# Performance work log

Hardware: AMD Instinct MI355X
Metric: run time of the kernel (lower is better)

Reference implementation:

```python
import jax, jax.numpy as jnp
import numpy as np


def _pairwise_sq_dists(p, t):
    # p: [N,3], t: [M,3] -> [N,M] squared euclidean distances
    # |p|^2 + |t|^2 - 2 p.t^T (avoids materializing [N,M,3])
    p2 = jnp.sum(p * p, axis=-1)  # [N]
    t2 = jnp.sum(t * t, axis=-1)  # [M]
    cross = jnp.einsum('nd,md->nm', p, t)  # [N,M]
    d = p2[:, None] + t2[None, :] - 2.0 * cross
    return jnp.maximum(d, 0.0)  # clamp tiny negatives from cancellation


def setup_inputs() -> dict:
    key = jax.random.key(0)
    k1, k2 = jax.random.split(key)
    N = 16384
    predict = jax.random.normal(k1, (1, N, 3), dtype=jnp.float32)
    target = jax.random.normal(k2, (1, N, 3), dtype=jnp.float32)
    return {"predict": predict, "target": target}


def reference(predict, target):
    # Faithful to forward: only the first batch element is used.
    p = predict[0]  # [N,3]
    t = target[0]   # [M,3]
    d = _pairwise_sq_dists(p, t)          # [N,M] squared distances
    dist1 = jnp.min(d, axis=1)            # nearest target for each predict pt
    dist2 = jnp.min(d, axis=0)            # nearest predict for each target pt
    loss = jnp.mean(dist1) + jnp.mean(dist2)
    return loss
```

## Files before the change

kernel.cpp:

```cpp
#include <hip/hip_runtime.h>


typedef short s16x8 __attribute__((ext_vector_type(8)));
typedef float f32x16 __attribute__((ext_vector_type(16)));

static __device__ __forceinline__ unsigned short f2bf(float f) {
    unsigned u = __float_as_uint(f);
    unsigned r = (u + 0x7FFFu + ((u >> 16) & 1u)) >> 16;
    return (unsigned short)r;
}
static __device__ __forceinline__ float bf2f(unsigned short h) {
    return __uint_as_float(((unsigned)h) << 16);
}
static __device__ __forceinline__ void split2(float v, unsigned short& h, unsigned short& l) {
    h = f2bf(v);
    l = f2bf(v - bf2f(h));
}

union Pack16 { unsigned short u[16]; uint4 v[2]; };

__global__ void prep_pack(const float* __restrict__ predict, const float* __restrict__ target,
                          unsigned short* __restrict__ ApP, unsigned short* __restrict__ BpP,
                          unsigned short* __restrict__ ApT, unsigned short* __restrict__ BpT,
                          int N)
{
    int i = blockIdx.x * blockDim.x + threadIdx.x;
    if (i >= 2 * N) return;
    const float* src = (i < N) ? predict : target;
    unsigned short* Ap = (i < N) ? ApP : ApT;
    unsigned short* Bp = (i < N) ? BpP : BpT;
    int j = (i < N) ? i : i - N;

    float x = src[3*j], y = src[3*j+1], z = src[3*j+2];
    float n2 = __builtin_fmaf(x, x, __builtin_fmaf(y, y, z*z));

    unsigned short xh,xl,yh,yl,zh,zl,nh,nl,qxh,qxl,qyh,qyl,qzh,qzl;
    split2(x, xh, xl); split2(y, yh, yl); split2(z, zh, zl); split2(n2, nh, nl);
    split2(-2.0f*x, qxh, qxl); split2(-2.0f*y, qyh, qyl); split2(-2.0f*z, qzh, qzl);
    const unsigned short one = f2bf(1.0f);

    Pack16 a, b;
    a.u[0]=xh; a.u[1]=xh; a.u[2]=xl; a.u[3]=xl;
    a.u[4]=yh; a.u[5]=yh; a.u[6]=yl; a.u[7]=yl;
    a.u[8]=zh; a.u[9]=zh; a.u[10]=zl; a.u[11]=zl;
    a.u[12]=nh; a.u[13]=nl; a.u[14]=one; a.u[15]=one;

    b.u[0]=qxh; b.u[1]=qxl; b.u[2]=qxh; b.u[3]=qxl;
    b.u[4]=qyh; b.u[5]=qyl; b.u[6]=qyh; b.u[7]=qyl;
    b.u[8]=qzh; b.u[9]=qzl; b.u[10]=qzh; b.u[11]=qzl;
    b.u[12]=one; b.u[13]=one; b.u[14]=nh; b.u[15]=nl;

    uint4* ad = (uint4*)(Ap + (size_t)j * 16);
    uint4* bd = (uint4*)(Bp + (size_t)j * 16);
    ad[0] = a.v[0]; ad[1] = a.v[1];
    bd[0] = b.v[0]; bd[1] = b.v[1];
}

#define CG 8

__global__ __launch_bounds__(256, 2) void chamfer_main(
    const unsigned short* __restrict__ ApP, const unsigned short* __restrict__ BpP,
    const unsigned short* __restrict__ ApT, const unsigned short* __restrict__ BpT,
    float* __restrict__ partials, int N)
{
    const int dir = blockIdx.z;
    const unsigned short* __restrict__ Ap = dir ? ApT : ApP;
    const unsigned short* __restrict__ Bp = dir ? BpP : BpT;
    float* __restrict__ pout = partials + (size_t)(dir * CG + blockIdx.y) * N;

    const int tid  = threadIdx.x;
    const int w    = tid >> 6;
    const int lane = tid & 63;
    const int lm   = lane & 31;
    const int lg   = lane >> 5;

    const int row0 = blockIdx.x * 256 + w * 64;

    const uint4* A4 = (const uint4*)Ap;
    s16x8 a0 = __builtin_bit_cast(s16x8, A4[(size_t)(row0      + lm) * 2 + lg]);
    s16x8 a1 = __builtin_bit_cast(s16x8, A4[(size_t)(row0 + 32 + lm) * 2 + lg]);

    float rm0[16], rm1[16];
    #pragma unroll
    for (int r = 0; r < 16; ++r) { rm0[r] = 3.0e38f; rm1[r] = 3.0e38f; }

    const f32x16 zc = {0.f,0.f,0.f,0.f,0.f,0.f,0.f,0.f,0.f,0.f,0.f,0.f,0.f,0.f,0.f,0.f};

    const int npt = N / CG;
    const int NT  = npt / 32;
    const uint4* bp = (const uint4*)Bp + (size_t)blockIdx.y * npt * 2 + lm * 2 + lg;

    uint4 c0 = bp[0];
    uint4 c1 = bp[64];
    const uint4* bnext = bp + 128;

    for (int t = 0; t < NT - 2; t += 2) {
        uint4 n0 = bnext[0];
        uint4 n1 = bnext[64];
        bnext += 128;
        s16x8 bA = __builtin_bit_cast(s16x8, c0);
        s16x8 bB = __builtin_bit_cast(s16x8, c1);
        f32x16 p0 = __builtin_amdgcn_mfma_f32_32x32x16_bf16(a0, bA, zc, 0, 0, 0);
        f32x16 q0 = __builtin_amdgcn_mfma_f32_32x32x16_bf16(a0, bB, zc, 0, 0, 0);
        f32x16 p1 = __builtin_amdgcn_mfma_f32_32x32x16_bf16(a1, bA, zc, 0, 0, 0);
        f32x16 q1 = __builtin_amdgcn_mfma_f32_32x32x16_bf16(a1, bB, zc, 0, 0, 0);
        #pragma unroll
        for (int r = 0; r < 16; ++r) {
            rm0[r] = fminf(fminf(rm0[r], p0[r]), q0[r]);
            rm1[r] = fminf(fminf(rm1[r], p1[r]), q1[r]);
        }
        c0 = n0; c1 = n1;
    }
    {
        s16x8 bA = __builtin_bit_cast(s16x8, c0);
        s16x8 bB = __builtin_bit_cast(s16x8, c1);
        f32x16 p0 = __builtin_amdgcn_mfma_f32_32x32x16_bf16(a0, bA, zc, 0, 0, 0);
        f32x16 q0 = __builtin_amdgcn_mfma_f32_32x32x16_bf16(a0, bB, zc, 0, 0, 0);
        f32x16 p1 = __builtin_amdgcn_mfma_f32_32x32x16_bf16(a1, bA, zc, 0, 0, 0);
        f32x16 q1 = __builtin_amdgcn_mfma_f32_32x32x16_bf16(a1, bB, zc, 0, 0, 0);
        #pragma unroll
        for (int r = 0; r < 16; ++r) {
            rm0[r] = fminf(fminf(rm0[r], p0[r]), q0[r]);
            rm1[r] = fminf(fminf(rm1[r], p1[r]), q1[r]);
        }
    }

    #pragma unroll
    for (int m = 1; m <= 16; m <<= 1) {
        #pragma unroll
        for (int r = 0; r < 16; ++r) {
            rm0[r] = fminf(rm0[r], __shfl_xor(rm0[r], m, 64));
            rm1[r] = fminf(rm1[r], __shfl_xor(rm1[r], m, 64));
        }
    }
    #pragma unroll
    for (int r = 0; r < 16; ++r) {
        int rl = (r & 3) + 8 * (r >> 2) + 4 * lg;
        if (lm == r) {
            pout[row0 +      rl] = rm0[r];
            pout[row0 + 32 + rl] = rm1[r];
        }
    }
}

__global__ void chamfer_reduce1(const float* __restrict__ partials,
                                double* __restrict__ bsum, int N)
{
    const int n4 = N >> 2;
    const float4* p4 = (const float4*)partials;
    double acc = 0.0;
    for (int i = blockIdx.x * blockDim.x + threadIdx.x; i < n4;
         i += gridDim.x * blockDim.x) {
        float4 m0 = p4[i];
        #pragma unroll
        for (int g = 1; g < CG; ++g) {
            float4 v = p4[(size_t)g * n4 + i];
            m0.x = fminf(m0.x, v.x); m0.y = fminf(m0.y, v.y);
            m0.z = fminf(m0.z, v.z); m0.w = fminf(m0.w, v.w);
        }
        float4 m1 = p4[(size_t)CG * n4 + i];
        #pragma unroll
        for (int g = CG + 1; g < 2 * CG; ++g) {
            float4 v = p4[(size_t)g * n4 + i];
            m1.x = fminf(m1.x, v.x); m1.y = fminf(m1.y, v.y);
            m1.z = fminf(m1.z, v.z); m1.w = fminf(m1.w, v.w);
        }
        acc += (double)fmaxf(m0.x, 0.0f) + (double)fmaxf(m0.y, 0.0f)
             + (double)fmaxf(m0.z, 0.0f) + (double)fmaxf(m0.w, 0.0f)
             + (double)fmaxf(m1.x, 0.0f) + (double)fmaxf(m1.y, 0.0f)
             + (double)fmaxf(m1.z, 0.0f) + (double)fmaxf(m1.w, 0.0f);
    }
    for (int off = 32; off; off >>= 1)
        acc += __shfl_down(acc, off, 64);
    __shared__ double sacc[4];
    const int wave = threadIdx.x >> 6, lane = threadIdx.x & 63;
    if (lane == 0) sacc[wave] = acc;
    __syncthreads();
    if (threadIdx.x == 0)
        bsum[blockIdx.x] = sacc[0] + sacc[1] + sacc[2] + sacc[3];
}

__global__ void chamfer_reduce2(const double* __restrict__ bsum,
                                float* __restrict__ out, int N, int nb)
{
    if (threadIdx.x == 0) {
        double t = 0.0;
        for (int i = 0; i < nb; ++i) t += bsum[i];
        out[0] = (float)(t / (double)N);
    }
}

extern "C" void kernel_launch(void* const* d_in, const int* in_sizes, int n_in,
                              void* d_out, int out_size, void* d_ws, size_t ws_size,
                              hipStream_t stream) {
    const float* predict = (const float*)d_in[0];
    const float* target  = (const float*)d_in[1];
    const int N = in_sizes[0] / 3;

    unsigned short* ws16 = (unsigned short*)d_ws;
    unsigned short* ApP = ws16;
    unsigned short* BpP = ws16 + (size_t)1 * N * 16;
    unsigned short* ApT = ws16 + (size_t)2 * N * 16;
    unsigned short* BpT = ws16 + (size_t)3 * N * 16;
    float* partials = (float*)(ws16 + (size_t)4 * N * 16);
    double* bsum = (double*)(partials + (size_t)2 * CG * N);

    prep_pack<<<dim3((2 * N + 255) / 256), dim3(256), 0, stream>>>(
        predict, target, ApP, BpP, ApT, BpT, N);

    dim3 grid(N / 256, CG, 2);
    chamfer_main<<<grid, dim3(256), 0, stream>>>(ApP, BpP, ApT, BpT, partials, N);

    chamfer_reduce1<<<dim3(16), dim3(256), 0, stream>>>(partials, bsum, N);
    chamfer_reduce2<<<dim3(1), dim3(64), 0, stream>>>(bsum, (float*)d_out, N, 16);
}
```

Before: 83.60 us.

## Fuse reductions into main kernel via atomicMin and last-block ticket

Drops the partials buffer and the two reduce kernels. Each block now atomicMins its clamped per-row minima, stored as uint bits, into a 2N array that prep_pack initialises, and the last block to finish (found with an atomic ticket) sums the array and writes the loss. The main loop is also unrolled to four B tiles per iteration with deeper prefetch. This cuts two kernel launches and the extra global traffic, at the cost of atomic contention, a serial final sum in one block, and higher register pressure.

New measurement: 146.6 us. 1.75x slower.

```diff
diff --git a/kernel.cpp b/kernel.cpp
--- a/kernel.cpp
+++ b/kernel.cpp
@@ -22,10 +22,14 @@
 __global__ void prep_pack(const float* __restrict__ predict, const float* __restrict__ target,
                           unsigned short* __restrict__ ApP, unsigned short* __restrict__ BpP,
                           unsigned short* __restrict__ ApT, unsigned short* __restrict__ BpT,
+                          unsigned* __restrict__ minbits, unsigned* __restrict__ ticket,
                           int N)
 {
     int i = blockIdx.x * blockDim.x + threadIdx.x;
+    if (i == 0) *ticket = 0u;
     if (i >= 2 * N) return;
+    minbits[i] = 0x7F7FFFFFu;
+
     const float* src = (i < N) ? predict : target;
     unsigned short* Ap = (i < N) ? ApP : ApT;
     unsigned short* Bp = (i < N) ? BpP : BpT;
@@ -61,12 +65,13 @@
 __global__ __launch_bounds__(256, 2) void chamfer_main(
     const unsigned short* __restrict__ ApP, const unsigned short* __restrict__ BpP,
     const unsigned short* __restrict__ ApT, const unsigned short* __restrict__ BpT,
-    float* __restrict__ partials, int N)
+    unsigned* __restrict__ minbits, unsigned* __restrict__ ticket,
+    float* __restrict__ out, int N)
 {
     const int dir = blockIdx.z;
     const unsigned short* __restrict__ Ap = dir ? ApT : ApP;
     const unsigned short* __restrict__ Bp = dir ? BpP : BpT;
-    float* __restrict__ pout = partials + (size_t)(dir * CG + blockIdx.y) * N;
+    unsigned* __restrict__ mout = minbits + (size_t)dir * N;
 
     const int tid  = threadIdx.x;
     const int w    = tid >> 6;
@@ -88,40 +93,69 @@
 
     const int npt = N / CG;
     const int NT  = npt / 32;
+    const int NQ  = NT / 4;
     const uint4* bp = (const uint4*)Bp + (size_t)blockIdx.y * npt * 2 + lm * 2 + lg;
 
-    uint4 c0 = bp[0];
-    uint4 c1 = bp[64];
-    const uint4* bnext = bp + 128;
-
-    for (int t = 0; t < NT - 2; t += 2) {
-        uint4 n0 = bnext[0];
-        uint4 n1 = bnext[64];
-        bnext += 128;
-        s16x8 bA = __builtin_bit_cast(s16x8, c0);
-        s16x8 bB = __builtin_bit_cast(s16x8, c1);
-        f32x16 p0 = __builtin_amdgcn_mfma_f32_32x32x16_bf16(a0, bA, zc, 0, 0, 0);
-        f32x16 q0 = __builtin_amdgcn_mfma_f32_32x32x16_bf16(a0, bB, zc, 0, 0, 0);
-        f32x16 p1 = __builtin_amdgcn_mfma_f32_32x32x16_bf16(a1, bA, zc, 0, 0, 0);
-        f32x16 q1 = __builtin_amdgcn_mfma_f32_32x32x16_bf16(a1, bB, zc, 0, 0, 0);
-        #pragma unroll
-        for (int r = 0; r < 16; ++r) {
-            rm0[r] = fminf(fminf(rm0[r], p0[r]), q0[r]);
-            rm1[r] = fminf(fminf(rm1[r], p1[r]), q1[r]);
-        }
-        c0 = n0; c1 = n1;
+    uint4 c0 = bp[0], c1 = bp[64], c2 = bp[128], c3 = bp[192];
+    const uint4* bn = bp + 256;
+
+    for (int t = 0; t < NQ - 1; ++t) {
+        uint4 n0 = bn[0], n1 = bn[64], n2 = bn[128], n3 = bn[192];
+        bn += 256;
+        {
+            s16x8 bA = __builtin_bit_cast(s16x8, c0);
+            s16x8 bB = __builtin_bit_cast(s16x8, c1);
+            f32x16 p0 = __builtin_amdgcn_mfma_f32_32x32x16_bf16(a0, bA, zc, 0, 0, 0);
+            f32x16 q0 = __builtin_amdgcn_mfma_f32_32x32x16_bf16(a0, bB, zc, 0, 0, 0);
+            f32x16 p1 = __builtin_amdgcn_mfma_f32_32x32x16_bf16(a1, bA, zc, 0, 0, 0);
+            f32x16 q1 = __builtin_amdgcn_mfma_f32_32x32x16_bf16(a1, bB, zc, 0, 0, 0);
+            #pragma unroll
+            for (int r = 0; r < 16; ++r) {
+                rm0[r] = fminf(fminf(rm0[r], p0[r]), q0[r]);
+                rm1[r] = fminf(fminf(rm1[r], p1[r]), q1[r]);
+            }
+        }
+        {
+            s16x8 bA = __builtin_bit_cast(s16x8, c2);
+            s16x8 bB = __builtin_bit_cast(s16x8, c3);
+            f32x16 p0 = __builtin_amdgcn_mfma_f32_32x32x16_bf16(a0, bA, zc, 0, 0, 0);
+            f32x16 q0 = __builtin_amdgcn_mfma_f32_32x32x16_bf16(a0, bB, zc, 0, 0, 0);
+            f32x16 p1 = __builtin_amdgcn_mfma_f32_32x32x16_bf16(a1, bA, zc, 0, 0, 0);
+            f32x16 q1 = __builtin_amdgcn_mfma_f32_32x32x16_bf16(a1, bB, zc, 0, 0, 0);
+            #pragma unroll
+            for (int r = 0; r < 16; ++r) {
+                rm0[r] = fminf(fminf(rm0[r], p0[r]), q0[r]);
+                rm1[r] = fminf(fminf(rm1[r], p1[r]), q1[r]);
+            }
+        }
+        c0 = n0; c1 = n1; c2 = n2; c3 = n3;
     }
     {
-        s16x8 bA = __builtin_bit_cast(s16x8, c0);
-        s16x8 bB = __builtin_bit_cast(s16x8, c1);
-        f32x16 p0 = __builtin_amdgcn_mfma_f32_32x32x16_bf16(a0, bA, zc, 0, 0, 0);
-        f32x16 q0 = __builtin_amdgcn_mfma_f32_32x32x16_bf16(a0, bB, zc, 0, 0, 0);
-        f32x16 p1 = __builtin_amdgcn_mfma_f32_32x32x16_bf16(a1, bA, zc, 0, 0, 0);
-        f32x16 q1 = __builtin_amdgcn_mfma_f32_32x32x16_bf16(a1, bB, zc, 0, 0, 0);
-        #pragma unroll
-        for (int r = 0; r < 16; ++r) {
-            rm0[r] = fminf(fminf(rm0[r], p0[r]), q0[r]);
-            rm1[r] = fminf(fminf(rm1[r], p1[r]), q1[r]);
+        {
+            s16x8 bA = __builtin_bit_cast(s16x8, c0);
+            s16x8 bB = __builtin_bit_cast(s16x8, c1);
+            f32x16 p0 = __builtin_amdgcn_mfma_f32_32x32x16_bf16(a0, bA, zc, 0, 0, 0);
+            f32x16 q0 = __builtin_amdgcn_mfma_f32_32x32x16_bf16(a0, bB, zc, 0, 0, 0);
+            f32x16 p1 = __builtin_amdgcn_mfma_f32_32x32x16_bf16(a1, bA, zc, 0, 0, 0);
+            f32x16 q1 = __builtin_amdgcn_mfma_f32_32x32x16_bf16(a1, bB, zc, 0, 0, 0);
+            #pragma unroll
+            for (int r = 0; r < 16; ++r) {
+                rm0[r] = fminf(fminf(rm0[r], p0[r]), q0[r]);
+                rm1[r] = fminf(fminf(rm1[r], p1[r]), q1[r]);
+            }
+        }
+        {
+            s16x8 bA = __builtin_bit_cast(s16x8, c2);
+            s16x8 bB = __builtin_bit_cast(s16x8, c3);
+            f32x16 p0 = __builtin_amdgcn_mfma_f32_32x32x16_bf16(a0, bA, zc, 0, 0, 0);
+            f32x16 q0 = __builtin_amdgcn_mfma_f32_32x32x16_bf16(a0, bB, zc, 0, 0, 0);
+            f32x16 p1 = __builtin_amdgcn_mfma_f32_32x32x16_bf16(a1, bA, zc, 0, 0, 0);
+            f32x16 q1 = __builtin_amdgcn_mfma_f32_32x32x16_bf16(a1, bB, zc, 0, 0, 0);
+            #pragma unroll
+            for (int r = 0; r < 16; ++r) {
+                rm0[r] = fminf(fminf(rm0[r], p0[r]), q0[r]);
+                rm1[r] = fminf(fminf(rm1[r], p1[r]), q1[r]);
+            }
         }
     }
 
@@ -137,57 +171,37 @@
     for (int r = 0; r < 16; ++r) {
         int rl = (r & 3) + 8 * (r >> 2) + 4 * lg;
         if (lm == r) {
-            pout[row0 +      rl] = rm0[r];
-            pout[row0 + 32 + rl] = rm1[r];
-        }
-    }
-}
-
-__global__ void chamfer_reduce1(const float* __restrict__ partials,
-                                double* __restrict__ bsum, int N)
-{
-    const int n4 = N >> 2;
-    const float4* p4 = (const float4*)partials;
+            atomicMin(&mout[row0 +      rl], __float_as_uint(fmaxf(rm0[r], 0.0f)));
+            atomicMin(&mout[row0 + 32 + rl], __float_as_uint(fmaxf(rm1[r], 0.0f)));
+        }
+    }
+
+    __threadfence();
+    __shared__ unsigned is_last;
+    if (tid == 0) {
+        unsigned total = gridDim.x * gridDim.y * gridDim.z;
+        unsigned old = atomicAdd(ticket, 1u);
+        is_last = (old == total - 1u) ? 1u : 0u;
+    }
+    __syncthreads();
+    if (!is_last) return;
+    __threadfence();
+
+    const uint4* mb4 = (const uint4*)minbits;
+    const int n4 = (2 * N) >> 2;
     double acc = 0.0;
-    for (int i = blockIdx.x * blockDim.x + threadIdx.x; i < n4;
-         i += gridDim.x * blockDim.x) {
-        float4 m0 = p4[i];
-        #pragma unroll
-        for (int g = 1; g < CG; ++g) {
-            float4 v = p4[(size_t)g * n4 + i];
-            m0.x = fminf(m0.x, v.x); m0.y = fminf(m0.y, v.y);
-            m0.z = fminf(m0.z, v.z); m0.w = fminf(m0.w, v.w);
-        }
-        float4 m1 = p4[(size_t)CG * n4 + i];
-        #pragma unroll
-        for (int g = CG + 1; g < 2 * CG; ++g) {
-            float4 v = p4[(size_t)g * n4 + i];
-            m1.x = fminf(m1.x, v.x); m1.y = fminf(m1.y, v.y);
-            m1.z = fminf(m1.z, v.z); m1.w = fminf(m1.w, v.w);
-        }
-        acc += (double)fmaxf(m0.x, 0.0f) + (double)fmaxf(m0.y, 0.0f)
-             + (double)fmaxf(m0.z, 0.0f) + (double)fmaxf(m0.w, 0.0f)
-             + (double)fmaxf(m1.x, 0.0f) + (double)fmaxf(m1.y, 0.0f)
-             + (double)fmaxf(m1.z, 0.0f) + (double)fmaxf(m1.w, 0.0f);
+    for (int i = tid; i < n4; i += 256) {
+        uint4 v = mb4[i];
+        acc += (double)__uint_as_float(v.x) + (double)__uint_as_float(v.y)
+             + (double)__uint_as_float(v.z) + (double)__uint_as_float(v.w);
     }
     for (int off = 32; off; off >>= 1)
         acc += __shfl_down(acc, off, 64);
     __shared__ double sacc[4];
-    const int wave = threadIdx.x >> 6, lane = threadIdx.x & 63;
-    if (lane == 0) sacc[wave] = acc;
+    if (lane == 0) sacc[w] = acc;
     __syncthreads();
-    if (threadIdx.x == 0)
-        bsum[blockIdx.x] = sacc[0] + sacc[1] + sacc[2] + sacc[3];
-}
-
-__global__ void chamfer_reduce2(const double* __restrict__ bsum,
-                                float* __restrict__ out, int N, int nb)
-{
-    if (threadIdx.x == 0) {
-        double t = 0.0;
-        for (int i = 0; i < nb; ++i) t += bsum[i];
-        out[0] = (float)(t / (double)N);
-    }
+    if (tid == 0)
+        out[0] = (float)((sacc[0] + sacc[1] + sacc[2] + sacc[3]) / (double)N);
 }
 
 extern "C" void kernel_launch(void* const* d_in, const int* in_sizes, int n_in,
@@ -202,15 +216,13 @@
     unsigned short* BpP = ws16 + (size_t)1 * N * 16;
     unsigned short* ApT = ws16 + (size_t)2 * N * 16;
     unsigned short* BpT = ws16 + (size_t)3 * N * 16;
-    float* partials = (float*)(ws16 + (size_t)4 * N * 16);
-    double* bsum = (double*)(partials + (size_t)2 * CG * N);
+    unsigned* minbits = (unsigned*)(ws16 + (size_t)4 * N * 16);
+    unsigned* ticket  = minbits + (size_t)2 * N;
 
     prep_pack<<<dim3((2 * N + 255) / 256), dim3(256), 0, stream>>>(
-        predict, target, ApP, BpP, ApT, BpT, N);
+        predict, target, ApP, BpP, ApT, BpT, minbits, ticket, N);
 
     dim3 grid(N / 256, CG, 2);
-    chamfer_main<<<grid, dim3(256), 0, stream>>>(ApP, BpP, ApT, BpT, partials, N);
-
-    chamfer_reduce1<<<dim3(16), dim3(256), 0, stream>>>(partials, bsum, N);
-    chamfer_reduce2<<<dim3(1), dim3(64), 0, stream>>>(bsum, (float*)d_out, N, 16);
-}
+    chamfer_main<<<grid, dim3(256), 0, stream>>>(
+        ApP, BpP, ApT, BpT, minbits, ticket, (float*)d_out, N);
+}
```
